# Performance work log

Measured on AMD Instinct MI355X. Metric: run time of the kernel, lower is better.

The kernel has to match this reference:

```python
import jax, jax.numpy as jnp
import numpy as np

T = 3          # hparams['T'] message-passing iterations
E = 100000     # num edges (rows of link_state)
M = 200000     # num message pairs
D = 128        # hidden dim of link_state / GRU units
H = 256        # Message MLP hidden width
G = 64         # num graphs


def setup_inputs() -> dict:
    key = jax.random.key(0)
    ks = jax.random.split(key, 16)
    s = 0.05
    inp = {
        'link_state': jax.random.normal(ks[0], (E, D), jnp.float32),
        'states_first': jax.random.randint(ks[1], (M,), 0, E),
        'states_second': jax.random.randint(ks[2], (M,), 0, E),
        'states_graph_ids': jnp.sort(jax.random.randint(ks[3], (E,), 0, G)),
        'sates_num_edges': E,
        # Message MLP: Dense(H, relu) -> Dense(D, relu)
        'mW1': jax.random.normal(ks[4], (2 * D, H), jnp.float32) * s,
        'mb1': jnp.zeros((H,), jnp.float32),
        'mW2': jax.random.normal(ks[5], (H, D), jnp.float32) * s,
        'mb2': jnp.zeros((D,), jnp.float32),
        # GRUCell (keras, reset_after=True): kernel [D,3D], recurrent [D,3D], bias [2,3D]
        'gru_kernel': jax.random.normal(ks[6], (D, 3 * D), jnp.float32) * s,
        'gru_recurrent': jax.random.normal(ks[7], (D, 3 * D), jnp.float32) * s,
        'gru_bias': jnp.zeros((2, 3 * D), jnp.float32),
        # Readout MLP: Dense(H, relu) -> Dense(H, relu) -> Dense(1)
        'rW1': jax.random.normal(ks[8], (D, H), jnp.float32) * s,
        'rb1': jnp.zeros((H,), jnp.float32),
        'rW2': jax.random.normal(ks[9], (H, H), jnp.float32) * s,
        'rb2': jnp.zeros((H,), jnp.float32),
        'rW3': jax.random.normal(ks[10], (H, 1), jnp.float32) * s,
        'rb3': jnp.zeros((1,), jnp.float32),
    }
    return inp


def _gru_step(x, h, kernel, recurrent, bias):
    # keras GRUCell with reset_after=True; gate order: z, r, h
    mx = x @ kernel + bias[0]          # [N, 3D]
    mh = h @ recurrent + bias[1]       # [N, 3D]
    xz, xr, xh = jnp.split(mx, 3, axis=-1)
    hz, hr, hh = jnp.split(mh, 3, axis=-1)
    z = jax.nn.sigmoid(xz + hz)
    r = jax.nn.sigmoid(xr + hr)
    hcand = jnp.tanh(xh + r * hh)
    return z * h + (1.0 - z) * hcand


def reference(link_state, states_first, states_second, states_graph_ids,
              sates_num_edges, mW1, mb1, mW2, mb2,
              gru_kernel, gru_recurrent, gru_bias,
              rW1, rb1, rW2, rb2, rW3, rb3):
    for _ in range(T):
        main_e = link_state[states_first]        # [M, D] gather
        neigh_e = link_state[states_second]      # [M, D] gather
        concat = jnp.concatenate([main_e, neigh_e], axis=1)  # [M, 2D]
        msg = jax.nn.relu(concat @ mW1 + mb1)
        msg = jax.nn.relu(msg @ mW2 + mb2)       # [M, D]
        edges_inputs = jax.ops.segment_sum(msg, states_second,
                                           num_segments=sates_num_edges)  # [E, D]
        link_state = _gru_step(edges_inputs, link_state,
                               gru_kernel, gru_recurrent, gru_bias)
    graph_state = jax.ops.segment_sum(link_state, states_graph_ids,
                                      num_segments=G)  # [G, D]
    r = jax.nn.relu(graph_state @ rW1 + rb1)
    r = jax.nn.relu(r @ rW2 + rb2)
    return r @ rW3 + rb3  # [G, 1]
```

## Files before the change

kernel.cpp:

```cpp
#include <hip/hip_runtime.h>

#define NUM_E 100000
#define NUM_M 200000
#define DIM   128
#define HID   256
#define NG    64
#define TITER 3
#define NB_SCAN 98
#define GS_ER 128

typedef __attribute__((ext_vector_type(8))) short bf16x8;
typedef __attribute__((ext_vector_type(4))) float f32x4;

__device__ __forceinline__ unsigned short f2bf(float f) {
  unsigned u = __float_as_uint(f);
  u += 0x7FFF + ((u >> 16) & 1);
  return (unsigned short)(u >> 16);
}
__device__ __forceinline__ float bf2f(unsigned short h) {
  return __uint_as_float(((unsigned)h) << 16);
}
__device__ __forceinline__ float sigmoidf_(float v) {
  return 1.f / (1.f + __expf(-v));
}
__device__ __forceinline__ float tanhf_(float u) {
  u = fminf(fmaxf(u, -15.f), 15.f);
  float ex = __expf(-2.f * u);
  return (1.f - ex) / (1.f + ex);
}
__device__ __forceinline__ float relu_(float v) { return fmaxf(v, 0.f); }

__device__ __forceinline__ void acc8(float* xs, bf16x8 v) {
  #pragma unroll
  for (int j = 0; j < 8; ++j) xs[j] += bf2f((unsigned short)v[j]);
}

__device__ __forceinline__ int swzm(int row, int col) {
  return row * 256 + (col ^ ((row & 7) << 3));
}
__device__ __forceinline__ int swzg(int row, int col) {
  return row * 128 + (col ^ ((row & 7) << 3));
}

#define MFMA(a, b, c) __builtin_amdgcn_mfma_f32_16x16x32_bf16((a), (b), (c), 0, 0, 0)

__global__ void hist_kernel(const int* __restrict__ second, int* __restrict__ counts,
                            float4* __restrict__ gs4) {
  int m = blockIdx.x * blockDim.x + threadIdx.x;
  if (m < NG * DIM / 4) gs4[m] = make_float4(0.f, 0.f, 0.f, 0.f);
  if (m < NUM_M) atomicAdd(&counts[second[m]], 1);
}

__global__ __launch_bounds__(256) void scan1_kernel(const int* __restrict__ counts,
                                                    int* __restrict__ partials) {
  __shared__ int sh[256];
  int b = blockIdx.x, t = threadIdx.x;
  int i0 = b * 1024 + t * 4;
  int c0 = (i0 + 0 < NUM_E) ? counts[i0 + 0] : 0;
  int c1 = (i0 + 1 < NUM_E) ? counts[i0 + 1] : 0;
  int c2 = (i0 + 2 < NUM_E) ? counts[i0 + 2] : 0;
  int c3 = (i0 + 3 < NUM_E) ? counts[i0 + 3] : 0;
  int tsum = c0 + c1 + c2 + c3;
  sh[t] = tsum;
  __syncthreads();
  for (int off = 1; off < 256; off <<= 1) {
    int v = (t >= off) ? sh[t - off] : 0;
    __syncthreads();
    sh[t] += v;
    __syncthreads();
  }
  if (t == 255) partials[b] = sh[255];
}

__global__ void scan2_kernel(const int* __restrict__ partials, int* __restrict__ base,
                             int* __restrict__ rowptr) {
  if (threadIdx.x == 0) {
    int run = 0;
    for (int b = 0; b < NB_SCAN; ++b) { base[b] = run; run += partials[b]; }
    rowptr[NUM_E] = NUM_M;
  }
}

__global__ __launch_bounds__(256) void scan3_kernel(const int* __restrict__ counts,
                                                    const int* __restrict__ base,
                                                    int* __restrict__ rowptr) {
  __shared__ int sh[256];
  int b = blockIdx.x, t = threadIdx.x;
  int i0 = b * 1024 + t * 4;
  int c0 = (i0 + 0 < NUM_E) ? counts[i0 + 0] : 0;
  int c1 = (i0 + 1 < NUM_E) ? counts[i0 + 1] : 0;
  int c2 = (i0 + 2 < NUM_E) ? counts[i0 + 2] : 0;
  int c3 = (i0 + 3 < NUM_E) ? counts[i0 + 3] : 0;
  int tsum = c0 + c1 + c2 + c3;
  sh[t] = tsum;
  __syncthreads();
  for (int off = 1; off < 256; off <<= 1) {
    int v = (t >= off) ? sh[t - off] : 0;
    __syncthreads();
    sh[t] += v;
    __syncthreads();
  }
  int p = base[b] + (sh[t] - tsum);
  if (i0 + 0 < NUM_E) rowptr[i0 + 0] = p;
  if (i0 + 1 < NUM_E) rowptr[i0 + 1] = p + c0;
  if (i0 + 2 < NUM_E) rowptr[i0 + 2] = p + c0 + c1;
  if (i0 + 3 < NUM_E) rowptr[i0 + 3] = p + c0 + c1 + c2;
}

__global__ void scatter_kernel(const int* __restrict__ second,
                               const int* __restrict__ rowptr,
                               int* __restrict__ cursor, int* __restrict__ order) {
  int m = blockIdx.x * blockDim.x + threadIdx.x;
  if (m < NUM_M) {
    int e = second[m];
    int pos = atomicAdd(&cursor[e], 1);
    int idx = rowptr[e] + pos;
    if (idx < rowptr[e + 1]) order[idx] = m;
  }
}

__device__ __forceinline__ void pack_range(
    const float* __restrict__ srcA, const float* __restrict__ srcB, int KrowsA,
    int N, int src_ld, int col_off, unsigned short* __restrict__ dst, int idx) {
  int l = idx & 63;
  int t = idx >> 6;
  int NF = N / 16;
  int nf = t % NF;
  int ks = t / NF;
  int n = nf * 16 + (l & 15) + col_off;
  int k0 = ks * 32 + (l >> 4) * 8;
  unsigned short o[8];
  #pragma unroll
  for (int j = 0; j < 8; ++j) {
    int k = k0 + j;
    const float* src = (k < KrowsA) ? (srcA + (size_t)k * src_ld)
                                    : (srcB + (size_t)(k - KrowsA) * src_ld);
    o[j] = f2bf(src[n]);
  }
  ushort4* d = (ushort4*)(dst + (size_t)idx * 8);
  d[0] = make_ushort4(o[0], o[1], o[2], o[3]);
  d[1] = make_ushort4(o[4], o[5], o[6], o[7]);
}

__global__ __launch_bounds__(256) void prep_kernel(
    const float4* __restrict__ ls4, ushort4* __restrict__ lsb4, int n4,
    const float* __restrict__ mW1, const float* __restrict__ mW2,
    const float* __restrict__ gk,  const float* __restrict__ gr,
    unsigned short* __restrict__ W1p,  unsigned short* __restrict__ W2p,
    unsigned short* __restrict__ Wzrp, unsigned short* __restrict__ Wkhp,
    unsigned short* __restrict__ Wrhp) {
  int i = blockIdx.x * 256 + threadIdx.x;
  if (i < n4) {
    float4 v = ls4[i];
    ushort4 o;
    o.x = f2bf(v.x); o.y = f2bf(v.y); o.z = f2bf(v.z); o.w = f2bf(v.w);
    lsb4[i] = o;
  }
  if      (i < 8192)  pack_range(mW1, mW1, 256, 256, 256, 0,   W1p,  i);
  else if (i < 12288) pack_range(mW2, mW2, 256, 128, 128, 0,   W2p,  i - 8192);
  else if (i < 20480) pack_range(gk,  gr,  128, 256, 384, 0,   Wzrp, i - 12288);
  else if (i < 22528) pack_range(gk,  gk,  128, 128, 384, 256, Wkhp, i - 20480);
  else if (i < 24576) pack_range(gr,  gr,  128, 128, 384, 256, Wrhp, i - 22528);
}

__global__ __launch_bounds__(512, 2) void msg_kernel(
    const unsigned short* __restrict__ lsb,
    const int* __restrict__ first, const int* __restrict__ second,
    const int* __restrict__ order,
    const unsigned short* __restrict__ W1p,
    const float* __restrict__ b1,
    const unsigned short* __restrict__ W2p,
    const float* __restrict__ b2,
    unsigned short* __restrict__ msgout)
{
  __shared__ unsigned short actL[2][32 * 256];
  __shared__ unsigned short h1s[2][32 * 256];

  const int tid  = threadIdx.x;
  const int wave = tid >> 6;
  const int lane = tid & 63;
  const int c    = lane & 15;
  const int quad = lane >> 4;

  const int sr  = tid >> 5;
  const int shf = (tid >> 4) & 1;
  const int si  = tid & 15;

  const bf16x8* W1f = (const bf16x8*)W1p;
  const bf16x8* W2f = (const bf16x8*)W2p;
  bf16x8 w1r[16];
  #pragma unroll
  for (int ks = 0; ks < 8; ++ks)
    #pragma unroll
    for (int i = 0; i < 2; ++i)
      w1r[ks * 2 + i] = W1f[(ks * 16 + wave * 2 + i) * 64 + lane];
  bf16x8 w2r[8];
  #pragma unroll
  for (int ks = 0; ks < 8; ++ks)
    w2r[ks] = W2f[(ks * 8 + wave) * 64 + lane];

  float4 b1v[2];
  #pragma unroll
  for (int i = 0; i < 2; ++i)
    b1v[i] = *(const float4*)(b1 + (wave * 2 + i) * 16 + quad * 4);
  float4 b2v = *(const float4*)(b2 + wave * 16 + quad * 4);

  const int nTiles = NUM_M / 32;
  const int stride = gridDim.x;
  int tile = blockIdx.x;
  if (tile >= nTiles) return;
  int parity = 0;

  {
    int m1 = order[tile * 32 + sr];
    int m2 = order[tile * 32 + 16 + sr];
    int e1 = shf ? second[m1] : first[m1];
    int e2 = shf ? second[m2] : first[m2];
    bf16x8 v1 = *(const bf16x8*)(lsb + (size_t)e1 * DIM + si * 8);
    bf16x8 v2 = *(const bf16x8*)(lsb + (size_t)e2 * DIM + si * 8);
    *(bf16x8*)&actL[0][swzm(sr,      shf * 128 + si * 8)] = v1;
    *(bf16x8*)&actL[0][swzm(sr + 16, shf * 128 + si * 8)] = v2;
  }
  int e1n = 0, e2n = 0;
  {
    int t1 = tile + stride;
    if (t1 < nTiles) {
      int m1 = order[t1 * 32 + sr];
      int m2 = order[t1 * 32 + 16 + sr];
      e1n = shf ? second[m1] : first[m1];
      e2n = shf ? second[m2] : first[m2];
    }
  }
  __syncthreads();

  while (true) {
    const int m0 = tile * 32;
    const int next  = tile + stride;
    const int next2 = next + stride;
    const bool have_next  = (next < nTiles);
    const bool have_next2 = (next2 < nTiles);

    bf16x8 sv1, sv2;
    if (have_next) {
      sv1 = *(const bf16x8*)(lsb + (size_t)e1n * DIM + si * 8);
      sv2 = *(const bf16x8*)(lsb + (size_t)e2n * DIM + si * 8);
    }
    int o1 = 0, o2 = 0;
    if (have_next2) {
      o1 = order[next2 * 32 + sr];
      o2 = order[next2 * 32 + 16 + sr];
    }

    const unsigned short* ab = &actL[parity][0];
    f32x4 accA[2], accB[2];
    #pragma unroll
    for (int i = 0; i < 2; ++i) { accA[i] = (f32x4)(0.f); accB[i] = (f32x4)(0.f); }
    #pragma unroll
    for (int ks = 0; ks < 8; ++ks) {
      bf16x8 bA = *(const bf16x8*)&ab[swzm(c,      ks * 32 + quad * 8)];
      bf16x8 bB = *(const bf16x8*)&ab[swzm(16 + c, ks * 32 + quad * 8)];
      #pragma unroll
      for (int i = 0; i < 2; ++i) {
        accA[i] = MFMA(w1r[ks * 2 + i], bA, accA[i]);
        accB[i] = MFMA(w1r[ks * 2 + i], bB, accB[i]);
      }
    }

    if (have_next2) {
      e1n = shf ? second[o1] : first[o1];
      e2n = shf ? second[o2] : first[o2];
    }

    if (have_next) {
      unsigned short* aw = &actL[parity ^ 1][0];
      *(bf16x8*)&aw[swzm(sr,      shf * 128 + si * 8)] = sv1;
      *(bf16x8*)&aw[swzm(sr + 16, shf * 128 + si * 8)] = sv2;
    }

    unsigned short* hb = &h1s[parity][0];
    #pragma unroll
    for (int i = 0; i < 2; ++i) {
      int n0 = (wave * 2 + i) * 16 + quad * 4;
      ushort4 pa, pb;
      pa.x = f2bf(relu_(accA[i][0] + b1v[i].x));
      pa.y = f2bf(relu_(accA[i][1] + b1v[i].y));
      pa.z = f2bf(relu_(accA[i][2] + b1v[i].z));
      pa.w = f2bf(relu_(accA[i][3] + b1v[i].w));
      pb.x = f2bf(relu_(accB[i][0] + b1v[i].x));
      pb.y = f2bf(relu_(accB[i][1] + b1v[i].y));
      pb.z = f2bf(relu_(accB[i][2] + b1v[i].z));
      pb.w = f2bf(relu_(accB[i][3] + b1v[i].w));
      *(ushort4*)&hb[swzm(c,      n0)] = pa;
      *(ushort4*)&hb[swzm(16 + c, n0)] = pb;
    }
    __syncthreads();

    f32x4 a2A = (f32x4)(0.f), a2B = (f32x4)(0.f);
    #pragma unroll
    for (int ks2 = 0; ks2 < 8; ++ks2) {
      bf16x8 bA = *(const bf16x8*)&hb[swzm(c,      ks2 * 32 + quad * 8)];
      bf16x8 bB = *(const bf16x8*)&hb[swzm(16 + c, ks2 * 32 + quad * 8)];
      a2A = MFMA(w2r[ks2], bA, a2A);
      a2B = MFMA(w2r[ks2], bB, a2B);
    }

    {
      int n0 = wave * 16 + quad * 4;
      ushort4 pa, pb;
      pa.x = f2bf(relu_(a2A[0] + b2v.x));
      pa.y = f2bf(relu_(a2A[1] + b2v.y));
      pa.z = f2bf(relu_(a2A[2] + b2v.z));
      pa.w = f2bf(relu_(a2A[3] + b2v.w));
      pb.x = f2bf(relu_(a2B[0] + b2v.x));
      pb.y = f2bf(relu_(a2B[1] + b2v.y));
      pb.z = f2bf(relu_(a2B[2] + b2v.z));
      pb.w = f2bf(relu_(a2B[3] + b2v.w));
      *(ushort4*)(msgout + (size_t)(m0 + c) * DIM + n0)      = pa;
      *(ushort4*)(msgout + (size_t)(m0 + 16 + c) * DIM + n0) = pb;
    }

    if (!have_next) break;
    tile = next;
    parity ^= 1;
  }
}

__device__ __forceinline__ ushort4 gru_gate(
    f32x4 az, f32x4 ar, f32x4 axh, f32x4 ahh, ushort4 hraw,
    float4 bz0, float4 br0, float4 bh0, float4 bz1, float4 br1, float4 bh1) {
  float ho[4] = { bf2f(hraw.x), bf2f(hraw.y), bf2f(hraw.z), bf2f(hraw.w) };
  const float* paz  = (const float*)&az;  const float* par  = (const float*)&ar;
  const float* paxh = (const float*)&axh; const float* pahh = (const float*)&ahh;
  const float* pz0 = (const float*)&bz0; const float* pr0 = (const float*)&br0;
  const float* ph0 = (const float*)&bh0; const float* pz1 = (const float*)&bz1;
  const float* pr1 = (const float*)&br1; const float* ph1 = (const float*)&bh1;
  unsigned short o[4];
  #pragma unroll
  for (int j = 0; j < 4; ++j) {
    float z  = sigmoidf_(paz[j] + pz0[j] + pz1[j]);
    float r  = sigmoidf_(par[j] + pr0[j] + pr1[j]);
    float hc = tanhf_(paxh[j] + ph0[j] + r * (pahh[j] + ph1[j]));
    o[j] = f2bf(z * ho[j] + (1.f - z) * hc);
  }
  return make_ushort4(o[0], o[1], o[2], o[3]);
}

__global__ __launch_bounds__(512, 2) void gru_kernel(
    const unsigned short* __restrict__ msgb,
    const int* __restrict__ rowptr,
    unsigned short* __restrict__ lsb,
    const unsigned short* __restrict__ Wzrp,
    const unsigned short* __restrict__ Wkhp,
    const unsigned short* __restrict__ Wrhp,
    const float* __restrict__ gb)
{
  __shared__ unsigned short xfL[2][32 * 128];
  __shared__ unsigned short hfL[2][32 * 128];

  const int tid  = threadIdx.x;
  const int wave = tid >> 6;
  const int lane = tid & 63;
  const int c    = lane & 15;
  const int quad = lane >> 4;

  const bf16x8* Wzrf = (const bf16x8*)Wzrp;
  const bf16x8* Wkhf = (const bf16x8*)Wkhp;
  const bf16x8* Wrhf = (const bf16x8*)Wrhp;
  bf16x8 wz[8], wr[8];
  #pragma unroll
  for (int ks = 0; ks < 8; ++ks) {
    wz[ks] = Wzrf[(ks * 16 + wave) * 64 + lane];
    wr[ks] = Wzrf[(ks * 16 + 8 + wave) * 64 + lane];
  }
  bf16x8 wxh[4], whh[4];
  #pragma unroll
  for (int ks = 0; ks < 4; ++ks) {
    wxh[ks] = Wkhf[(ks * 8 + wave) * 64 + lane];
    whh[ks] = Wrhf[(ks * 8 + wave) * 64 + lane];
  }

  const float4* gbv = (const float4*)gb;
  const int q4 = wave * 4 + quad;
  const float4 b0z = gbv[q4],      b0r = gbv[32 + q4],  b0h = gbv[64 + q4];
  const float4 b1z = gbv[96 + q4], b1r = gbv[128 + q4], b1h = gbv[160 + q4];

  const int el = wave * 4 + (lane >> 4);
  const int li = lane & 15;

  const int nTiles = NUM_E / 32;
  const int stride = gridDim.x;
  int tile = blockIdx.x;
  if (tile >= nTiles) return;
  int par = 0;

  {
    const int e  = tile * 32 + el;
    const int rs = rowptr[e], re = rowptr[e + 1];
    float xs[8];
    #pragma unroll
    for (int j = 0; j < 8; ++j) xs[j] = 0.f;
    bf16x8 hrow = *(const bf16x8*)(lsb + (size_t)e * DIM + li * 8);
    for (int p0 = rs; p0 < re; p0 += 8) {
      const int pm = re - 1;
      bf16x8 tv[8];
      #pragma unroll
      for (int k = 0; k < 8; ++k)
        tv[k] = *(const bf16x8*)(msgb + (size_t)min(p0 + k, pm) * DIM + li * 8);
      #pragma unroll
      for (int k = 0; k < 8; ++k)
        if (p0 + k < re) acc8(xs, tv[k]);
    }
    bf16x8 xv;
    #pragma unroll
    for (int j = 0; j < 8; ++j) xv[j] = (short)f2bf(xs[j]);
    *(bf16x8*)&xfL[0][swzg(el, li * 8)] = xv;
    *(bf16x8*)&hfL[0][swzg(el, li * 8)] = hrow;
  }
  int rs1 = 0, re1 = 0;
  if (tile + stride < nTiles) {
    const int e1 = (tile + stride) * 32 + el;
    rs1 = rowptr[e1]; re1 = rowptr[e1 + 1];
  }
  __syncthreads();

  while (true) {
    const int nextT = tile + stride;
    const bool have_next  = (nextT < nTiles);
    const bool have_next2 = (nextT + stride < nTiles);

    bf16x8 r0, r1, r2, r3, r4, r5, r6, r7, hrow;
    if (have_next) {
      const int e1 = nextT * 32 + el;
      const int pc = min(max(re1 - 1, rs1), NUM_M - 1);
      r0 = *(const bf16x8*)(msgb + (size_t)min(rs1 + 0, pc) * DIM + li * 8);
      r1 = *(const bf16x8*)(msgb + (size_t)min(rs1 + 1, pc) * DIM + li * 8);
      r2 = *(const bf16x8*)(msgb + (size_t)min(rs1 + 2, pc) * DIM + li * 8);
      r3 = *(const bf16x8*)(msgb + (size_t)min(rs1 + 3, pc) * DIM + li * 8);
      r4 = *(const bf16x8*)(msgb + (size_t)min(rs1 + 4, pc) * DIM + li * 8);
      r5 = *(const bf16x8*)(msgb + (size_t)min(rs1 + 5, pc) * DIM + li * 8);
      r6 = *(const bf16x8*)(msgb + (size_t)min(rs1 + 6, pc) * DIM + li * 8);
      r7 = *(const bf16x8*)(msgb + (size_t)min(rs1 + 7, pc) * DIM + li * 8);
      hrow = *(const bf16x8*)(lsb + (size_t)e1 * DIM + li * 8);
    }
    int rs2 = 0, re2 = 0;
    if (have_next2) {
      const int e2 = (nextT + stride) * 32 + el;
      rs2 = rowptr[e2]; re2 = rowptr[e2 + 1];
    }

    const unsigned short* xb = &xfL[par][0];
    const unsigned short* hb = &hfL[par][0];
    f32x4 zA = (f32x4)(0.f), zB = (f32x4)(0.f);
    f32x4 rA = (f32x4)(0.f), rB = (f32x4)(0.f);
    f32x4 xhA = (f32x4)(0.f), xhB = (f32x4)(0.f);
    f32x4 hhA = (f32x4)(0.f), hhB = (f32x4)(0.f);
    #pragma unroll
    for (int ks = 0; ks < 4; ++ks) {
      bf16x8 xA = *(const bf16x8*)&xb[swzg(c,      ks * 32 + quad * 8)];
      bf16x8 xB = *(const bf16x8*)&xb[swzg(16 + c, ks * 32 + quad * 8)];
      bf16x8 hA = *(const bf16x8*)&hb[swzg(c,      ks * 32 + quad * 8)];
      bf16x8 hB = *(const bf16x8*)&hb[swzg(16 + c, ks * 32 + quad * 8)];
      zA  = MFMA(wz[ks],     xA, zA);   zB  = MFMA(wz[ks],     xB, zB);
      rA  = MFMA(wr[ks],     xA, rA);   rB  = MFMA(wr[ks],     xB, rB);
      zA  = MFMA(wz[4 + ks], hA, zA);   zB  = MFMA(wz[4 + ks], hB, zB);
      rA  = MFMA(wr[4 + ks], hA, rA);   rB  = MFMA(wr[4 + ks], hB, rB);
      xhA = MFMA(wxh[ks],    xA, xhA);  xhB = MFMA(wxh[ks],    xB, xhB);
      hhA = MFMA(whh[ks],    hA, hhA);  hhB = MFMA(whh[ks],    hB, hhB);
    }
    {
      const int n0 = wave * 16 + quad * 4;
      ushort4 hrawA = *(const ushort4*)&hb[swzg(c,      n0)];
      ushort4 hrawB = *(const ushort4*)&hb[swzg(16 + c, n0)];
      ushort4 pkA = gru_gate(zA, rA, xhA, hhA, hrawA, b0z, b0r, b0h, b1z, b1r, b1h);
      ushort4 pkB = gru_gate(zB, rB, xhB, hhB, hrawB, b0z, b0r, b0h, b1z, b1r, b1h);
      *(ushort4*)(lsb + (size_t)(tile * 32 + c) * DIM + n0)      = pkA;
      *(ushort4*)(lsb + (size_t)(tile * 32 + 16 + c) * DIM + n0) = pkB;
    }

    if (have_next) {
      float xs[8];
      #pragma unroll
      for (int j = 0; j < 8; ++j) xs[j] = 0.f;
      if (rs1 + 0 < re1) acc8(xs, r0);
      if (rs1 + 1 < re1) acc8(xs, r1);
      if (rs1 + 2 < re1) acc8(xs, r2);
      if (rs1 + 3 < re1) acc8(xs, r3);
      if (rs1 + 4 < re1) acc8(xs, r4);
      if (rs1 + 5 < re1) acc8(xs, r5);
      if (rs1 + 6 < re1) acc8(xs, r6);
      if (rs1 + 7 < re1) acc8(xs, r7);
      for (int p0 = rs1 + 8; p0 < re1; p0 += 8) {
        const int pm = re1 - 1;
        bf16x8 tv[8];
        #pragma unroll
        for (int k = 0; k < 8; ++k)
          tv[k] = *(const bf16x8*)(msgb + (size_t)min(p0 + k, pm) * DIM + li * 8);
        #pragma unroll
        for (int k = 0; k < 8; ++k)
          if (p0 + k < re1) acc8(xs, tv[k]);
      }
      bf16x8 xv;
      #pragma unroll
      for (int j = 0; j < 8; ++j) xv[j] = (short)f2bf(xs[j]);
      *(bf16x8*)&xfL[par ^ 1][swzg(el, li * 8)] = xv;
      *(bf16x8*)&hfL[par ^ 1][swzg(el, li * 8)] = hrow;
    }
    __syncthreads();
    if (!have_next) break;
    tile = nextT;
    par ^= 1;
    rs1 = rs2;
    re1 = re2;
  }
}

__global__ __launch_bounds__(256) void graph_sum_kernel(
    const unsigned short* __restrict__ lsb, const int* __restrict__ gids,
    float* __restrict__ gs) {
  const int t = threadIdx.x;
  const int d = t & 127;
  const int half = t >> 7;
  const int e0 = blockIdx.x * GS_ER;
  const int e1 = min(e0 + GS_ER, NUM_E);
  float acc = 0.f;
  int cur = -1;
  for (int e = e0 + half; e < e1; e += 2) {
    int g = gids[e];
    if (g != cur) {
      if (cur >= 0) atomicAdd(&gs[cur * DIM + d], acc);
      acc = 0.f;
      cur = g;
    }
    acc += bf2f(lsb[(size_t)e * DIM + d]);
  }
  if (cur >= 0) atomicAdd(&gs[cur * DIM + d], acc);
}

__global__ __launch_bounds__(256) void readout_kernel(
    const float* __restrict__ gs,
    const float* __restrict__ rW1, const float* __restrict__ rb1,
    const float* __restrict__ rW2, const float* __restrict__ rb2,
    const float* __restrict__ rW3, const float* __restrict__ rb3,
    float* __restrict__ out) {
  __shared__ float shg[DIM];
  __shared__ float sh1[HID];
  __shared__ float red[HID];
  int g = blockIdx.x, c = threadIdx.x;
  if (c < DIM) shg[c] = gs[g * DIM + c];
  __syncthreads();
  float s = rb1[c];
  for (int k = 0; k < DIM; ++k) s += shg[k] * rW1[k * HID + c];
  sh1[c] = relu_(s);
  __syncthreads();
  s = rb2[c];
  for (int k = 0; k < HID; ++k) s += sh1[k] * rW2[k * HID + c];
  red[c] = relu_(s) * rW3[c];
  __syncthreads();
  for (int off = 128; off > 0; off >>= 1) {
    if (c < off) red[c] += red[c + off];
    __syncthreads();
  }
  if (c == 0) out[g] = red[0] + rb3[0];
}

extern "C" void kernel_launch(void* const* d_in, const int* in_sizes, int n_in,
                              void* d_out, int out_size, void* d_ws, size_t ws_size,
                              hipStream_t stream) {
  float* ls          = (float*)d_in[0];
  const int* first   = (const int*)d_in[1];
  const int* second  = (const int*)d_in[2];
  const int* gids    = (const int*)d_in[3];
  const float* mW1   = (const float*)d_in[5];
  const float* mb1   = (const float*)d_in[6];
  const float* mW2   = (const float*)d_in[7];
  const float* mb2   = (const float*)d_in[8];
  const float* gk    = (const float*)d_in[9];
  const float* gr    = (const float*)d_in[10];
  const float* gb    = (const float*)d_in[11];
  const float* rW1   = (const float*)d_in[12];
  const float* rb1   = (const float*)d_in[13];
  const float* rW2   = (const float*)d_in[14];
  const float* rb2   = (const float*)d_in[15];
  const float* rW3   = (const float*)d_in[16];
  const float* rb3   = (const float*)d_in[17];
  float* out = (float*)d_out;

  char* w = (char*)d_ws;
  unsigned short* msgb = (unsigned short*)w;    w += (size_t)NUM_M * DIM * 2;
  unsigned short* lsb  = (unsigned short*)w;    w += (size_t)NUM_E * DIM * 2;
  float* gs    = (float*)w;                     w += NG * DIM * 4;
  int* counts  = (int*)w;                       w += NUM_E * 4;
  int* cursor  = (int*)w;                       w += NUM_E * 4;
  int* rowptr  = (int*)w;                       w += (NUM_E + 4) * 4;
  int* order   = (int*)w;                       w += NUM_M * 4;
  int* partials= (int*)w;                       w += NB_SCAN * 4;
  int* basep   = (int*)w;                       w += NB_SCAN * 4;
  unsigned short* W1p  = (unsigned short*)w;    w += 256 * 256 * 2;
  unsigned short* W2p  = (unsigned short*)w;    w += 256 * 128 * 2;
  unsigned short* Wzrp = (unsigned short*)w;    w += 256 * 256 * 2;
  unsigned short* Wkhp = (unsigned short*)w;    w += 128 * 128 * 2;
  unsigned short* Wrhp = (unsigned short*)w;    w += 128 * 128 * 2;

  const int n4 = NUM_E * DIM / 4;
  prep_kernel<<<(n4 + 255) / 256, 256, 0, stream>>>(
      (const float4*)ls, (ushort4*)lsb, n4, mW1, mW2, gk, gr,
      W1p, W2p, Wzrp, Wkhp, Wrhp);

  hipMemsetAsync(counts, 0, 2 * (size_t)NUM_E * 4, stream);
  hist_kernel<<<(NUM_M + 255) / 256, 256, 0, stream>>>(second, counts, (float4*)gs);
  scan1_kernel<<<NB_SCAN, 256, 0, stream>>>(counts, partials);
  scan2_kernel<<<1, 64, 0, stream>>>(partials, basep, rowptr);
  scan3_kernel<<<NB_SCAN, 256, 0, stream>>>(counts, basep, rowptr);
  scatter_kernel<<<(NUM_M + 255) / 256, 256, 0, stream>>>(second, rowptr, cursor, order);

  for (int t = 0; t < TITER; ++t) {
    msg_kernel<<<256, 512, 0, stream>>>(lsb, first, second, order, W1p, mb1, W2p, mb2, msgb);
    gru_kernel<<<256, 512, 0, stream>>>(msgb, rowptr, lsb, Wzrp, Wkhp, Wrhp, gb);
  }
  graph_sum_kernel<<<(NUM_E + GS_ER - 1) / GS_ER, 256, 0, stream>>>(lsb, gids, gs);
  readout_kernel<<<NG, HID, 0, stream>>>(gs, rW1, rb1, rW2, rb2, rW3, rb3, out);
}
```

Measured before the change: 530.0 us.

## Enlarge message MLP tile from 32 to 64 rows per block iteration

The persistent message kernel now processes 64 message rows per tile instead of 32. Each wave reuses its register-resident W1/W2 fragments across four 16-row MFMA sub-tiles and prefetches four gathered rows per thread, which amortizes barriers and loop overhead over more work. Shared memory doubles to 128 KB per block under launch_bounds(512,2), so occupancy may drop, and the larger accumulator arrays raise register pressure.

```diff
diff --git a/kernel.cpp b/kernel.cpp
--- a/kernel.cpp
+++ b/kernel.cpp
@@ -8,6 +8,7 @@
 #define TITER 3
 #define NB_SCAN 98
 #define GS_ER 128
+#define TM    64
 
 typedef __attribute__((ext_vector_type(8))) short bf16x8;
 typedef __attribute__((ext_vector_type(4))) float f32x4;
@@ -173,8 +174,8 @@
     const float* __restrict__ b2,
     unsigned short* __restrict__ msgout)
 {
-  __shared__ unsigned short actL[2][32 * 256];
-  __shared__ unsigned short h1s[2][32 * 256];
+  __shared__ unsigned short actL[2][TM * 256];
+  __shared__ unsigned short h1s[2][TM * 256];
 
   const int tid  = threadIdx.x;
   const int wave = tid >> 6;
@@ -205,118 +206,120 @@
     b1v[i] = *(const float4*)(b1 + (wave * 2 + i) * 16 + quad * 4);
   float4 b2v = *(const float4*)(b2 + wave * 16 + quad * 4);
 
-  const int nTiles = NUM_M / 32;
+  const int nTiles = NUM_M / TM;
   const int stride = gridDim.x;
   int tile = blockIdx.x;
   if (tile >= nTiles) return;
   int parity = 0;
 
   {
-    int m1 = order[tile * 32 + sr];
-    int m2 = order[tile * 32 + 16 + sr];
-    int e1 = shf ? second[m1] : first[m1];
-    int e2 = shf ? second[m2] : first[m2];
-    bf16x8 v1 = *(const bf16x8*)(lsb + (size_t)e1 * DIM + si * 8);
-    bf16x8 v2 = *(const bf16x8*)(lsb + (size_t)e2 * DIM + si * 8);
-    *(bf16x8*)&actL[0][swzm(sr,      shf * 128 + si * 8)] = v1;
-    *(bf16x8*)&actL[0][swzm(sr + 16, shf * 128 + si * 8)] = v2;
-  }
-  int e1n = 0, e2n = 0;
+    #pragma unroll
+    for (int k = 0; k < 4; ++k) {
+      int m = order[tile * TM + sr + k * 16];
+      int e = shf ? second[m] : first[m];
+      bf16x8 v = *(const bf16x8*)(lsb + (size_t)e * DIM + si * 8);
+      *(bf16x8*)&actL[0][swzm(sr + k * 16, shf * 128 + si * 8)] = v;
+    }
+  }
+  int en[4] = {0, 0, 0, 0};
   {
     int t1 = tile + stride;
     if (t1 < nTiles) {
-      int m1 = order[t1 * 32 + sr];
-      int m2 = order[t1 * 32 + 16 + sr];
-      e1n = shf ? second[m1] : first[m1];
-      e2n = shf ? second[m2] : first[m2];
+      #pragma unroll
+      for (int k = 0; k < 4; ++k) {
+        int m = order[t1 * TM + sr + k * 16];
+        en[k] = shf ? second[m] : first[m];
+      }
     }
   }
   __syncthreads();
 
   while (true) {
-    const int m0 = tile * 32;
+    const int m0 = tile * TM;
     const int next  = tile + stride;
     const int next2 = next + stride;
     const bool have_next  = (next < nTiles);
     const bool have_next2 = (next2 < nTiles);
 
-    bf16x8 sv1, sv2;
+    bf16x8 sv[4];
     if (have_next) {
-      sv1 = *(const bf16x8*)(lsb + (size_t)e1n * DIM + si * 8);
-      sv2 = *(const bf16x8*)(lsb + (size_t)e2n * DIM + si * 8);
-    }
-    int o1 = 0, o2 = 0;
+      #pragma unroll
+      for (int k = 0; k < 4; ++k)
+        sv[k] = *(const bf16x8*)(lsb + (size_t)en[k] * DIM + si * 8);
+    }
+    int o[4] = {0, 0, 0, 0};
     if (have_next2) {
-      o1 = order[next2 * 32 + sr];
-      o2 = order[next2 * 32 + 16 + sr];
+      #pragma unroll
+      for (int k = 0; k < 4; ++k)
+        o[k] = order[next2 * TM + sr + k * 16];
     }
 
     const unsigned short* ab = &actL[parity][0];
-    f32x4 accA[2], accB[2];
-    #pragma unroll
-    for (int i = 0; i < 2; ++i) { accA[i] = (f32x4)(0.f); accB[i] = (f32x4)(0.f); }
+    f32x4 acc[4][2];
+    #pragma unroll
+    for (int s = 0; s < 4; ++s) { acc[s][0] = (f32x4)(0.f); acc[s][1] = (f32x4)(0.f); }
     #pragma unroll
     for (int ks = 0; ks < 8; ++ks) {
-      bf16x8 bA = *(const bf16x8*)&ab[swzm(c,      ks * 32 + quad * 8)];
-      bf16x8 bB = *(const bf16x8*)&ab[swzm(16 + c, ks * 32 + quad * 8)];
-      #pragma unroll
-      for (int i = 0; i < 2; ++i) {
-        accA[i] = MFMA(w1r[ks * 2 + i], bA, accA[i]);
-        accB[i] = MFMA(w1r[ks * 2 + i], bB, accB[i]);
+      #pragma unroll
+      for (int s = 0; s < 4; ++s) {
+        bf16x8 b = *(const bf16x8*)&ab[swzm(s * 16 + c, ks * 32 + quad * 8)];
+        acc[s][0] = MFMA(w1r[ks * 2 + 0], b, acc[s][0]);
+        acc[s][1] = MFMA(w1r[ks * 2 + 1], b, acc[s][1]);
       }
     }
 
     if (have_next2) {
-      e1n = shf ? second[o1] : first[o1];
-      e2n = shf ? second[o2] : first[o2];
+      #pragma unroll
+      for (int k = 0; k < 4; ++k)
+        en[k] = shf ? second[o[k]] : first[o[k]];
     }
 
     if (have_next) {
       unsigned short* aw = &actL[parity ^ 1][0];
-      *(bf16x8*)&aw[swzm(sr,      shf * 128 + si * 8)] = sv1;
-      *(bf16x8*)&aw[swzm(sr + 16, shf * 128 + si * 8)] = sv2;
+      #pragma unroll
+      for (int k = 0; k < 4; ++k)
+        *(bf16x8*)&aw[swzm(sr + k * 16, shf * 128 + si * 8)] = sv[k];
     }
 
     unsigned short* hb = &h1s[parity][0];
     #pragma unroll
     for (int i = 0; i < 2; ++i) {
       int n0 = (wave * 2 + i) * 16 + quad * 4;
-      ushort4 pa, pb;
-      pa.x = f2bf(relu_(accA[i][0] + b1v[i].x));
-      pa.y = f2bf(relu_(accA[i][1] + b1v[i].y));
-      pa.z = f2bf(relu_(accA[i][2] + b1v[i].z));
-      pa.w = f2bf(relu_(accA[i][3] + b1v[i].w));
-      pb.x = f2bf(relu_(accB[i][0] + b1v[i].x));
-      pb.y = f2bf(relu_(accB[i][1] + b1v[i].y));
-      pb.z = f2bf(relu_(accB[i][2] + b1v[i].z));
-      pb.w = f2bf(relu_(accB[i][3] + b1v[i].w));
-      *(ushort4*)&hb[swzm(c,      n0)] = pa;
-      *(ushort4*)&hb[swzm(16 + c, n0)] = pb;
+      #pragma unroll
+      for (int s = 0; s < 4; ++s) {
+        ushort4 pk;
+        pk.x = f2bf(relu_(acc[s][i][0] + b1v[i].x));
+        pk.y = f2bf(relu_(acc[s][i][1] + b1v[i].y));
+        pk.z = f2bf(relu_(acc[s][i][2] + b1v[i].z));
+        pk.w = f2bf(relu_(acc[s][i][3] + b1v[i].w));
+        *(ushort4*)&hb[swzm(s * 16 + c, n0)] = pk;
+      }
     }
     __syncthreads();
 
-    f32x4 a2A = (f32x4)(0.f), a2B = (f32x4)(0.f);
+    f32x4 a2[4];
+    #pragma unroll
+    for (int s = 0; s < 4; ++s) a2[s] = (f32x4)(0.f);
     #pragma unroll
     for (int ks2 = 0; ks2 < 8; ++ks2) {
-      bf16x8 bA = *(const bf16x8*)&hb[swzm(c,      ks2 * 32 + quad * 8)];
-      bf16x8 bB = *(const bf16x8*)&hb[swzm(16 + c, ks2 * 32 + quad * 8)];
-      a2A = MFMA(w2r[ks2], bA, a2A);
-      a2B = MFMA(w2r[ks2], bB, a2B);
+      #pragma unroll
+      for (int s = 0; s < 4; ++s) {
+        bf16x8 b = *(const bf16x8*)&hb[swzm(s * 16 + c, ks2 * 32 + quad * 8)];
+        a2[s] = MFMA(w2r[ks2], b, a2[s]);
+      }
     }
 
     {
       int n0 = wave * 16 + quad * 4;
-      ushort4 pa, pb;
-      pa.x = f2bf(relu_(a2A[0] + b2v.x));
-      pa.y = f2bf(relu_(a2A[1] + b2v.y));
-      pa.z = f2bf(relu_(a2A[2] + b2v.z));
-      pa.w = f2bf(relu_(a2A[3] + b2v.w));
-      pb.x = f2bf(relu_(a2B[0] + b2v.x));
-      pb.y = f2bf(relu_(a2B[1] + b2v.y));
-      pb.z = f2bf(relu_(a2B[2] + b2v.z));
-      pb.w = f2bf(relu_(a2B[3] + b2v.w));
-      *(ushort4*)(msgout + (size_t)(m0 + c) * DIM + n0)      = pa;
-      *(ushort4*)(msgout + (size_t)(m0 + 16 + c) * DIM + n0) = pb;
+      #pragma unroll
+      for (int s = 0; s < 4; ++s) {
+        ushort4 pk;
+        pk.x = f2bf(relu_(a2[s][0] + b2v.x));
+        pk.y = f2bf(relu_(a2[s][1] + b2v.y));
+        pk.z = f2bf(relu_(a2[s][2] + b2v.z));
+        pk.w = f2bf(relu_(a2[s][3] + b2v.w));
+        *(ushort4*)(msgout + (size_t)(m0 + s * 16 + c) * DIM + n0) = pk;
+      }
     }
 
     if (!have_next) break;
```

Result: faster. 495.4 us (-6.5%).
